# Kernel tuning notes

Measured on AMD Instinct MI355X. Metric: run time of the kernel, lower is better.

The kernel has to match this reference:

```python
import jax, jax.numpy as jnp
import numpy as np

NEG_INF = -1e6  # matches d2l masked_softmax fill value


def masked_softmax(scores, valid_len):
    # scores: [B, Q, K]; valid_len: [B] int — keys at positions >= valid_len[b] are masked
    K = scores.shape[-1]
    mask = jnp.arange(K, dtype=jnp.int32)[None, None, :] < valid_len[:, None, None]
    scores = jnp.where(mask, scores, NEG_INF)
    return jax.nn.softmax(scores, axis=-1)


def setup_inputs() -> dict:
    key = jax.random.key(0)
    k1, k2, k3, k4 = jax.random.split(key, 4)
    B, S, D = 8, 4096, 64
    query = jax.random.normal(k1, (B, S, D), dtype=jnp.float32)
    key_t = jax.random.normal(k2, (B, S, D), dtype=jnp.float32)
    value = jax.random.normal(k3, (B, S, D), dtype=jnp.float32)
    valid_len = jax.random.randint(k4, (B,), 1, S + 1, dtype=jnp.int32)
    return {"query": query, "key": key_t, "value": value, "valid_len": valid_len}


def reference(query, key, value, valid_len):
    d = query.shape[-1]
    # [B, Q, K] score matrix (the module materializes it explicitly)
    scores = jnp.einsum("bqd,bkd->bqk", query, key) / jnp.sqrt(jnp.float32(d))
    attn = masked_softmax(scores, valid_len)
    # dropout p=0.0 (eval): identity
    out = jnp.einsum("bqk,bkd->bqd", attn, value)
    return out
```

## Files before the change

### kernel.cpp

```cpp
#include <hip/hip_runtime.h>
#include <stdint.h>


constexpr int BB = 8;
constexpr int SS = 4096;
constexpr int DH = 64;
constexpr int CH = 32;
constexpr int NKT = SS / CH;
constexpr int TILE_SHORTS = 8192;
constexpr int NTILE = BB * (SS / 128);
constexpr int NSL = 4;
constexpr int SC = NKT / NSL;

typedef short  bfrag  __attribute__((ext_vector_type(8)));
typedef float  f32x16 __attribute__((ext_vector_type(16)));
typedef unsigned int uvec4 __attribute__((ext_vector_type(4)));

__device__ __forceinline__ unsigned short f2bf(float x) {
  unsigned u = __builtin_bit_cast(unsigned, x);
  u += 0x7fffu + ((u >> 16) & 1u);
  return (unsigned short)(u >> 16);
}
__device__ __forceinline__ float bf2f(unsigned short h) {
  return __builtin_bit_cast(float, ((unsigned)h) << 16);
}

__global__ __launch_bounds__(256) void prepack(
    const float* __restrict__ K, const float* __restrict__ V,
    short* __restrict__ ws) {
  const int b  = blockIdx.x >> 7;
  const int kt = blockIdx.x & 127;
  const int t  = threadIdx.x;
  short* tile = ws + (size_t)(b * NKT + kt) * TILE_SHORTS;

  {
    const int d8 = t >> 5, key = t & 31;
    const float* src = K + ((size_t)b * SS + kt * CH + key) * DH + d8 * 8;
    float4 a = ((const float4*)src)[0];
    float4 c = ((const float4*)src)[1];
    float v[8] = {a.x, a.y, a.z, a.w, c.x, c.y, c.z, c.w};
    bfrag hi, lo;
#pragma unroll
    for (int j = 0; j < 8; ++j) {
      unsigned short h = f2bf(v[j]);
      hi[j] = (short)h;
      lo[j] = (short)f2bf(v[j] - bf2f(h));
    }
    *(bfrag*)(tile + t * 8)        = hi;
    *(bfrag*)(tile + 2048 + t * 8) = lo;
  }
  {
    const int k8 = t >> 6, d = t & 63;
    const float* src = V + ((size_t)b * SS + kt * CH + k8 * 8) * DH + d;
    bfrag hi, lo;
#pragma unroll
    for (int j = 0; j < 8; ++j) {
      float x = src[j * DH];
      unsigned short h = f2bf(x);
      hi[j] = (short)h;
      lo[j] = (short)f2bf(x - bf2f(h));
    }
    *(bfrag*)(tile + 4096 + t * 8) = hi;
    *(bfrag*)(tile + 6144 + t * 8) = lo;
  }
}

__global__ __launch_bounds__(256, 4) void attn_mfma(
    const float* __restrict__ Q, const short* __restrict__ wsT,
    const int* __restrict__ VL, float* __restrict__ Out,
    float* __restrict__ part_o, float* __restrict__ part_ml, int nsl, int sc) {
  __shared__ __align__(16) short sKV[2][TILE_SHORTS];

  const int blk = blockIdx.x;
  const int b  = (blk >> 3) & 7;
  const int qs = ((blk >> 6) << 3) | (blk & 7);
  const int qt = qs >> 2;
  const int slice = qs & 3;
  const int tid = threadIdx.x;
  const int w   = tid >> 6;
  const int l   = tid & 63;
  const int hi5 = l >> 5;
  const int l31 = l & 31;

  const int vlen = VL[b];
  const int nch  = (vlen + CH - 1) / CH;
  int nact = (nch + sc - 1) / sc;
  if (nact > nsl) nact = nsl;
  if (slice >= nact) return;
  const int c_lo = slice * sc;
  const int c_hi = min(c_lo + sc, nch);
  const int nchS = c_hi - c_lo;

  bfrag qh[4], ql[4];
  {
    const float* qsrc = Q + ((size_t)b * SS + qt * 128 + w * 32 + l31) * DH;
#pragma unroll
    for (int dt = 0; dt < 4; ++dt) {
      const float* pp = qsrc + dt * 16 + hi5 * 8;
      float4 a = ((const float4*)pp)[0];
      float4 c = ((const float4*)pp)[1];
      float v[8] = {a.x, a.y, a.z, a.w, c.x, c.y, c.z, c.w};
#pragma unroll
      for (int j = 0; j < 8; ++j) {
        float x = v[j] * 0.125f;
        unsigned short h = f2bf(x);
        qh[dt][j] = (short)h;
        ql[dt][j] = (short)f2bf(x - bf2f(h));
      }
    }
  }

  f32x16 o0, o1;
#pragma unroll
  for (int r = 0; r < 16; ++r) { o0[r] = 0.f; o1[r] = 0.f; }
  float m = -1e30f, lsum = 0.f;

  const short* tbase = wsT + (size_t)b * NKT * TILE_SHORTS;

  auto stage = [&](int ci, int buf) {
    const short* g = tbase + (size_t)ci * TILE_SHORTS;
#pragma unroll
    for (int j = 0; j < 4; ++j) {
      __builtin_amdgcn_global_load_lds(
          (const __attribute__((address_space(1))) void*)(g + (j * 256 + tid) * 8),
          (__attribute__((address_space(3))) void*)(&sKV[buf][(j * 256 + tid) * 8]),
          16, 0, 0);
    }
  };

  stage(c_lo, 0);

  for (int t = 0; t < nchS; ++t) {
    __syncthreads();
    const int ci  = c_lo + t;
    const int cur = t & 1;
    if (t + 1 < nchS) stage(ci + 1, cur ^ 1);
    const short* t0 = &sKV[cur][0];

    f32x16 accA, accB;
#pragma unroll
    for (int r = 0; r < 16; ++r) { accA[r] = 0.f; accB[r] = 0.f; }
#pragma unroll
    for (int dt = 0; dt < 4; ++dt) {
      bfrag kh = *(const bfrag*)(t0 + ((2 * dt + hi5) * 32 + l31) * 8);
      bfrag kl = *(const bfrag*)(t0 + 2048 + ((2 * dt + hi5) * 32 + l31) * 8);
      accA = __builtin_amdgcn_mfma_f32_32x32x16_bf16(kh, qh[dt], accA, 0, 0, 0);
      if (dt < 2)
        accA = __builtin_amdgcn_mfma_f32_32x32x16_bf16(kh, ql[dt], accA, 0, 0, 0);
      else
        accB = __builtin_amdgcn_mfma_f32_32x32x16_bf16(kh, ql[dt], accB, 0, 0, 0);
      accB = __builtin_amdgcn_mfma_f32_32x32x16_bf16(kl, qh[dt], accB, 0, 0, 0);
    }
    float s[16];
#pragma unroll
    for (int r = 0; r < 16; ++r) s[r] = accA[r] + accB[r];

    const int c0 = ci * CH;
    if (c0 + CH > vlen) {
#pragma unroll
      for (int r = 0; r < 16; ++r) {
        int key = c0 + (r & 3) + 8 * (r >> 2) + 4 * hi5;
        if (key >= vlen) s[r] = -1e30f;
      }
    }

    float cmax = s[0];
#pragma unroll
    for (int r = 1; r < 16; ++r) cmax = fmaxf(cmax, s[r]);
    cmax = fmaxf(cmax, __shfl_xor(cmax, 32));

    if (__any((int)(cmax > m + 8.0f))) {
      float mn = fmaxf(m, cmax);
      float sc2 = __expf(m - mn);
      m = mn;
      lsum *= sc2;
#pragma unroll
      for (int r = 0; r < 16; ++r) {
        float s2 = __shfl(sc2, (r & 3) + 8 * (r >> 2) + 4 * hi5);
        o0[r] *= s2;
        o1[r] *= s2;
      }
    }

    float ps = 0.f;
#pragma unroll
    for (int r = 0; r < 16; ++r) {
      s[r] = __expf(s[r] - m);
      ps += s[r];
    }
    ps += __shfl_xor(ps, 32);
    lsum += ps;

    unsigned wh[8], wl2[8];
#pragma unroll
    for (int i = 0; i < 8; ++i) {
      float p0 = s[2 * i], p1 = s[2 * i + 1];
      unsigned hw;
      asm("v_cvt_pk_bf16_f32 %0, %1, %2" : "=v"(hw) : "v"(p0), "v"(p1));
      float h0 = __builtin_bit_cast(float, hw << 16);
      float h1 = __builtin_bit_cast(float, hw & 0xffff0000u);
      float r0 = p0 - h0, r1 = p1 - h1;
      unsigned lw;
      asm("v_cvt_pk_bf16_f32 %0, %1, %2" : "=v"(lw) : "v"(r0), "v"(r1));
      wh[i] = hw;
      wl2[i] = lw;
    }
    asm("v_permlane32_swap_b32 %0, %1" : "+v"(wh[0]), "+v"(wh[2]));
    asm("v_permlane32_swap_b32 %0, %1" : "+v"(wh[1]), "+v"(wh[3]));
    asm("v_permlane32_swap_b32 %0, %1" : "+v"(wh[4]), "+v"(wh[6]));
    asm("v_permlane32_swap_b32 %0, %1" : "+v"(wh[5]), "+v"(wh[7]));
    asm("v_permlane32_swap_b32 %0, %1" : "+v"(wl2[0]), "+v"(wl2[2]));
    asm("v_permlane32_swap_b32 %0, %1" : "+v"(wl2[1]), "+v"(wl2[3]));
    asm("v_permlane32_swap_b32 %0, %1" : "+v"(wl2[4]), "+v"(wl2[6]));
    asm("v_permlane32_swap_b32 %0, %1" : "+v"(wl2[5]), "+v"(wl2[7]));
    bfrag ph[2], pl[2];
    {
      uvec4 u0 = {wh[0], wh[1], wh[2], wh[3]};
      uvec4 u1 = {wh[4], wh[5], wh[6], wh[7]};
      uvec4 u2 = {wl2[0], wl2[1], wl2[2], wl2[3]};
      uvec4 u3 = {wl2[4], wl2[5], wl2[6], wl2[7]};
      ph[0] = __builtin_bit_cast(bfrag, u0);
      ph[1] = __builtin_bit_cast(bfrag, u1);
      pl[0] = __builtin_bit_cast(bfrag, u2);
      pl[1] = __builtin_bit_cast(bfrag, u3);
    }

#pragma unroll
    for (int ks = 0; ks < 2; ++ks) {
      const int vo = ((2 * ks + hi5) * 64 + l31) * 8;
      bfrag vh0 = *(const bfrag*)(t0 + 4096 + vo);
      bfrag vl0 = *(const bfrag*)(t0 + 6144 + vo);
      bfrag vh1 = *(const bfrag*)(t0 + 4096 + vo + 256);
      bfrag vl1 = *(const bfrag*)(t0 + 6144 + vo + 256);
      o0 = __builtin_amdgcn_mfma_f32_32x32x16_bf16(ph[ks], vh0, o0, 0, 0, 0);
      o0 = __builtin_amdgcn_mfma_f32_32x32x16_bf16(ph[ks], vl0, o0, 0, 0, 0);
      o0 = __builtin_amdgcn_mfma_f32_32x32x16_bf16(pl[ks], vh0, o0, 0, 0, 0);
      o1 = __builtin_amdgcn_mfma_f32_32x32x16_bf16(ph[ks], vh1, o1, 0, 0, 0);
      o1 = __builtin_amdgcn_mfma_f32_32x32x16_bf16(ph[ks], vl1, o1, 0, 0, 0);
      o1 = __builtin_amdgcn_mfma_f32_32x32x16_bf16(pl[ks], vh1, o1, 0, 0, 0);
    }
  }

  const float linv = 1.0f / lsum;
  if (nact == 1) {
    float* ob = Out + ((size_t)b * SS + qt * 128 + w * 32) * DH;
#pragma unroll
    for (int r = 0; r < 16; ++r) {
      int row = (r & 3) + 8 * (r >> 2) + 4 * hi5;
      float li = __shfl(linv, row);
      ob[row * DH + l31]      = o0[r] * li;
      ob[row * DH + 32 + l31] = o1[r] * li;
    }
  } else {
    const size_t base = (size_t)((b * 32 + qt) * nsl + slice);
    float* po = part_o + base * 8192 + w * 32 * 64;
#pragma unroll
    for (int r = 0; r < 16; ++r) {
      int row = (r & 3) + 8 * (r >> 2) + 4 * hi5;
      po[row * 64 + l31]      = o0[r];
      po[row * 64 + 32 + l31] = o1[r];
    }
    if (hi5 == 0) {
      part_ml[base * 256 + (w * 32 + l31) * 2 + 0] = m;
      part_ml[base * 256 + (w * 32 + l31) * 2 + 1] = lsum;
    }
  }
}

__global__ __launch_bounds__(256) void combine(
    const float* __restrict__ part_o, const float* __restrict__ part_ml,
    const int* __restrict__ VL, float* __restrict__ Out, int nsl, int sc) {
  const int blk = blockIdx.x;
  const int b = blk & 7, qt = blk >> 3;
  const int vlen = VL[b];
  const int nch = (vlen + CH - 1) / CH;
  int nact = (nch + sc - 1) / sc;
  if (nact > nsl) nact = nsl;
  if (nact < 2) return;
  const int row = threadIdx.x >> 1;
  const int seg = (threadIdx.x & 1) * 32;
  const size_t base = (size_t)(b * 32 + qt) * nsl;

  float ms[4], ls[4];
  float M = -1e30f;
#pragma unroll
  for (int s = 0; s < 4; ++s) {
    if (s < nact) {
      ms[s] = part_ml[(base + s) * 256 + row * 2 + 0];
      ls[s] = part_ml[(base + s) * 256 + row * 2 + 1];
      M = fmaxf(M, ms[s]);
    } else { ms[s] = -1e30f; ls[s] = 0.f; }
  }
  float L = 0.f;
#pragma unroll
  for (int s = 0; s < 4; ++s) {
    ms[s] = __expf(ms[s] - M);
    L += ms[s] * ls[s];
  }
  const float linv = 1.0f / L;

  float4 acc[8];
#pragma unroll
  for (int j = 0; j < 8; ++j) acc[j] = make_float4(0.f, 0.f, 0.f, 0.f);
#pragma unroll
  for (int s = 0; s < 4; ++s) {
    if (s < nact) {
      const float4* po =
          (const float4*)(part_o + (base + s) * 8192 + row * 64 + seg);
#pragma unroll
      for (int j = 0; j < 8; ++j) {
        float4 v = po[j];
        acc[j].x += ms[s] * v.x;
        acc[j].y += ms[s] * v.y;
        acc[j].z += ms[s] * v.z;
        acc[j].w += ms[s] * v.w;
      }
    }
  }
  float4* op = (float4*)(Out + ((size_t)b * SS + qt * 128 + row) * DH + seg);
#pragma unroll
  for (int j = 0; j < 8; ++j) {
    acc[j].x *= linv; acc[j].y *= linv; acc[j].z *= linv; acc[j].w *= linv;
    op[j] = acc[j];
  }
}

__global__ __launch_bounds__(256) void attn_naive(
    const float* __restrict__ Q, const float* __restrict__ K,
    const float* __restrict__ V, const int* __restrict__ VL,
    float* __restrict__ Out) {
  const int row = blockIdx.x * 256 + threadIdx.x;
  const int b = row >> 12;
  const int vlen = VL[b];
  const float* q = Q + (size_t)row * DH;
  float qr[DH];
#pragma unroll
  for (int d = 0; d < DH; ++d) qr[d] = q[d] * 0.125f;
  float m = -1e30f, ls = 0.f, o[DH];
#pragma unroll
  for (int d = 0; d < DH; ++d) o[d] = 0.f;
  const float* Kb = K + (size_t)b * SS * DH;
  const float* Vb = V + (size_t)b * SS * DH;
  for (int k = 0; k < vlen; ++k) {
    float sc = 0.f;
    for (int d = 0; d < DH; ++d) sc += qr[d] * Kb[(size_t)k * DH + d];
    if (sc > m) {
      float scale = __expf(m - sc);
      m = sc;
      ls *= scale;
      for (int d = 0; d < DH; ++d) o[d] *= scale;
    }
    float pv = __expf(sc - m);
    ls += pv;
    for (int d = 0; d < DH; ++d) o[d] += pv * Vb[(size_t)k * DH + d];
  }
  for (int d = 0; d < DH; ++d) Out[(size_t)row * DH + d] = o[d] / ls;
}

extern "C" void kernel_launch(void* const* d_in, const int* in_sizes, int n_in,
                              void* d_out, int out_size, void* d_ws,
                              size_t ws_size, hipStream_t stream) {
  const float* Q  = (const float*)d_in[0];
  const float* K  = (const float*)d_in[1];
  const float* V  = (const float*)d_in[2];
  const int*   VL = (const int*)d_in[3];
  float* Out = (float*)d_out;

  const size_t pack_bytes = (size_t)BB * NKT * TILE_SHORTS * sizeof(short);
  const size_t po_bytes   = (size_t)NTILE * NSL * 8192 * sizeof(float);
  const size_t pml_bytes  = (size_t)NTILE * NSL * 256 * sizeof(float);
  const size_t need_split = pack_bytes + po_bytes + pml_bytes;

  if (ws_size >= need_split) {
    short* pack = (short*)d_ws;
    float* po   = (float*)((char*)d_ws + pack_bytes);
    float* pml  = (float*)((char*)d_ws + pack_bytes + po_bytes);
    prepack<<<dim3(BB * NKT), dim3(256), 0, stream>>>(K, V, pack);
    attn_mfma<<<dim3(NTILE * NSL), dim3(256), 0, stream>>>(
        Q, pack, VL, Out, po, pml, NSL, SC);
    combine<<<dim3(NTILE), dim3(256), 0, stream>>>(po, pml, VL, Out, NSL, SC);
  } else if (ws_size >= pack_bytes) {
    short* pack = (short*)d_ws;
    prepack<<<dim3(BB * NKT), dim3(256), 0, stream>>>(K, V, pack);
    attn_mfma<<<dim3(NTILE), dim3(256), 0, stream>>>(
        Q, pack, VL, Out, (float*)d_ws, (float*)d_ws, 1, NKT);
  } else {
    attn_naive<<<dim3(BB * SS / 256), dim3(256), 0, stream>>>(Q, K, V, VL, Out);
  }
}
```

Measured before the change: 171.9 us.

## Balance split-K slices per batch and halve query tile per block

Each batch's valid key chunks are now divided evenly across the four split-K slices, instead of using a fixed slice length that leaves short batches on fewer blocks. The query tile shrinks from 128 to 64 rows, giving 128-thread blocks and twice as many blocks. The combine kernel now always merges all slices, with the partial buffers resized to match. This targets load imbalance from varying valid lengths across batches. In exchange, K/V tiles are streamed twice as often per query row, and the combine pass runs even when splitting is not needed.

```diff
diff --git a/kernel.cpp b/kernel.cpp
--- a/kernel.cpp
+++ b/kernel.cpp
@@ -8,9 +8,8 @@
 constexpr int CH = 32;
 constexpr int NKT = SS / CH;
 constexpr int TILE_SHORTS = 8192;
-constexpr int NTILE = BB * (SS / 128);
+constexpr int TPB = BB * (SS / 64);
 constexpr int NSL = 4;
-constexpr int SC = NKT / NSL;
 
 typedef short  bfrag  __attribute__((ext_vector_type(8)));
 typedef float  f32x16 __attribute__((ext_vector_type(16)));
@@ -65,17 +64,17 @@
   }
 }
 
-__global__ __launch_bounds__(256, 4) void attn_mfma(
+__global__ __launch_bounds__(128, 4) void attn_mfma(
     const float* __restrict__ Q, const short* __restrict__ wsT,
     const int* __restrict__ VL, float* __restrict__ Out,
-    float* __restrict__ part_o, float* __restrict__ part_ml, int nsl, int sc) {
+    float* __restrict__ part_o, float* __restrict__ part_ml, int nsl) {
   __shared__ __align__(16) short sKV[2][TILE_SHORTS];
 
   const int blk = blockIdx.x;
-  const int b  = (blk >> 3) & 7;
-  const int qs = ((blk >> 6) << 3) | (blk & 7);
-  const int qt = qs >> 2;
-  const int slice = qs & 3;
+  const int b    = blk & 7;
+  const int rest = blk >> 3;
+  const int qt    = rest / nsl;
+  const int slice = rest % nsl;
   const int tid = threadIdx.x;
   const int w   = tid >> 6;
   const int l   = tid & 63;
@@ -84,16 +83,13 @@
 
   const int vlen = VL[b];
   const int nch  = (vlen + CH - 1) / CH;
-  int nact = (nch + sc - 1) / sc;
-  if (nact > nsl) nact = nsl;
-  if (slice >= nact) return;
-  const int c_lo = slice * sc;
-  const int c_hi = min(c_lo + sc, nch);
+  const int c_lo = slice * nch / nsl;
+  const int c_hi = (slice + 1) * nch / nsl;
   const int nchS = c_hi - c_lo;
 
   bfrag qh[4], ql[4];
   {
-    const float* qsrc = Q + ((size_t)b * SS + qt * 128 + w * 32 + l31) * DH;
+    const float* qsrc = Q + ((size_t)b * SS + qt * 64 + w * 32 + l31) * DH;
 #pragma unroll
     for (int dt = 0; dt < 4; ++dt) {
       const float* pp = qsrc + dt * 16 + hi5 * 8;
@@ -120,15 +116,15 @@
   auto stage = [&](int ci, int buf) {
     const short* g = tbase + (size_t)ci * TILE_SHORTS;
 #pragma unroll
-    for (int j = 0; j < 4; ++j) {
+    for (int j = 0; j < 8; ++j) {
       __builtin_amdgcn_global_load_lds(
-          (const __attribute__((address_space(1))) void*)(g + (j * 256 + tid) * 8),
-          (__attribute__((address_space(3))) void*)(&sKV[buf][(j * 256 + tid) * 8]),
+          (const __attribute__((address_space(1))) void*)(g + (j * 128 + tid) * 8),
+          (__attribute__((address_space(3))) void*)(&sKV[buf][(j * 128 + tid) * 8]),
           16, 0, 0);
     }
   };
 
-  stage(c_lo, 0);
+  if (nchS > 0) stage(c_lo, 0);
 
   for (int t = 0; t < nchS; ++t) {
     __syncthreads();
@@ -241,9 +237,9 @@
     }
   }
 
-  const float linv = 1.0f / lsum;
-  if (nact == 1) {
-    float* ob = Out + ((size_t)b * SS + qt * 128 + w * 32) * DH;
+  if (nsl == 1) {
+    const float linv = 1.0f / lsum;
+    float* ob = Out + ((size_t)b * SS + qt * 64 + w * 32) * DH;
 #pragma unroll
     for (int r = 0; r < 16; ++r) {
       int row = (r & 3) + 8 * (r >> 2) + 4 * hi5;
@@ -252,8 +248,8 @@
       ob[row * DH + 32 + l31] = o1[r] * li;
     }
   } else {
-    const size_t base = (size_t)((b * 32 + qt) * nsl + slice);
-    float* po = part_o + base * 8192 + w * 32 * 64;
+    const size_t base = (size_t)((b * 64 + qt) * nsl + slice);
+    float* po = part_o + base * 4096 + w * 32 * 64;
 #pragma unroll
     for (int r = 0; r < 16; ++r) {
       int row = (r & 3) + 8 * (r >> 2) + 4 * hi5;
@@ -261,65 +257,56 @@
       po[row * 64 + 32 + l31] = o1[r];
     }
     if (hi5 == 0) {
-      part_ml[base * 256 + (w * 32 + l31) * 2 + 0] = m;
-      part_ml[base * 256 + (w * 32 + l31) * 2 + 1] = lsum;
+      part_ml[base * 128 + (w * 32 + l31) * 2 + 0] = m;
+      part_ml[base * 128 + (w * 32 + l31) * 2 + 1] = lsum;
     }
   }
 }
 
 __global__ __launch_bounds__(256) void combine(
     const float* __restrict__ part_o, const float* __restrict__ part_ml,
-    const int* __restrict__ VL, float* __restrict__ Out, int nsl, int sc) {
+    float* __restrict__ Out, int nsl) {
   const int blk = blockIdx.x;
   const int b = blk & 7, qt = blk >> 3;
-  const int vlen = VL[b];
-  const int nch = (vlen + CH - 1) / CH;
-  int nact = (nch + sc - 1) / sc;
-  if (nact > nsl) nact = nsl;
-  if (nact < 2) return;
-  const int row = threadIdx.x >> 1;
-  const int seg = (threadIdx.x & 1) * 32;
-  const size_t base = (size_t)(b * 32 + qt) * nsl;
-
-  float ms[4], ls[4];
+  const int row = threadIdx.x >> 2;
+  const int seg = (threadIdx.x & 3) * 16;
+  const size_t base = (size_t)(b * 64 + qt) * nsl;
+
+  float ms[NSL], ls[NSL];
   float M = -1e30f;
 #pragma unroll
-  for (int s = 0; s < 4; ++s) {
-    if (s < nact) {
-      ms[s] = part_ml[(base + s) * 256 + row * 2 + 0];
-      ls[s] = part_ml[(base + s) * 256 + row * 2 + 1];
-      M = fmaxf(M, ms[s]);
-    } else { ms[s] = -1e30f; ls[s] = 0.f; }
+  for (int s = 0; s < NSL; ++s) {
+    ms[s] = part_ml[(base + s) * 128 + row * 2 + 0];
+    ls[s] = part_ml[(base + s) * 128 + row * 2 + 1];
+    M = fmaxf(M, ms[s]);
   }
   float L = 0.f;
 #pragma unroll
-  for (int s = 0; s < 4; ++s) {
+  for (int s = 0; s < NSL; ++s) {
     ms[s] = __expf(ms[s] - M);
     L += ms[s] * ls[s];
   }
   const float linv = 1.0f / L;
 
-  float4 acc[8];
-#pragma unroll
-  for (int j = 0; j < 8; ++j) acc[j] = make_float4(0.f, 0.f, 0.f, 0.f);
-#pragma unroll
-  for (int s = 0; s < 4; ++s) {
-    if (s < nact) {
-      const float4* po =
-          (const float4*)(part_o + (base + s) * 8192 + row * 64 + seg);
-#pragma unroll
-      for (int j = 0; j < 8; ++j) {
-        float4 v = po[j];
-        acc[j].x += ms[s] * v.x;
-        acc[j].y += ms[s] * v.y;
-        acc[j].z += ms[s] * v.z;
-        acc[j].w += ms[s] * v.w;
-      }
-    }
-  }
-  float4* op = (float4*)(Out + ((size_t)b * SS + qt * 128 + row) * DH + seg);
-#pragma unroll
-  for (int j = 0; j < 8; ++j) {
+  float4 acc[4];
+#pragma unroll
+  for (int j = 0; j < 4; ++j) acc[j] = make_float4(0.f, 0.f, 0.f, 0.f);
+#pragma unroll
+  for (int s = 0; s < NSL; ++s) {
+    const float4* po =
+        (const float4*)(part_o + (base + s) * 4096 + row * 64 + seg);
+#pragma unroll
+    for (int j = 0; j < 4; ++j) {
+      float4 v = po[j];
+      acc[j].x += ms[s] * v.x;
+      acc[j].y += ms[s] * v.y;
+      acc[j].z += ms[s] * v.z;
+      acc[j].w += ms[s] * v.w;
+    }
+  }
+  float4* op = (float4*)(Out + ((size_t)b * SS + qt * 64 + row) * DH + seg);
+#pragma unroll
+  for (int j = 0; j < 4; ++j) {
     acc[j].x *= linv; acc[j].y *= linv; acc[j].z *= linv; acc[j].w *= linv;
     op[j] = acc[j];
   }
@@ -367,8 +354,8 @@
   float* Out = (float*)d_out;
 
   const size_t pack_bytes = (size_t)BB * NKT * TILE_SHORTS * sizeof(short);
-  const size_t po_bytes   = (size_t)NTILE * NSL * 8192 * sizeof(float);
-  const size_t pml_bytes  = (size_t)NTILE * NSL * 256 * sizeof(float);
+  const size_t po_bytes   = (size_t)TPB * NSL * 4096 * sizeof(float);
+  const size_t pml_bytes  = (size_t)TPB * NSL * 128 * sizeof(float);
   const size_t need_split = pack_bytes + po_bytes + pml_bytes;
 
   if (ws_size >= need_split) {
@@ -376,14 +363,14 @@
     float* po   = (float*)((char*)d_ws + pack_bytes);
     float* pml  = (float*)((char*)d_ws + pack_bytes + po_bytes);
     prepack<<<dim3(BB * NKT), dim3(256), 0, stream>>>(K, V, pack);
-    attn_mfma<<<dim3(NTILE * NSL), dim3(256), 0, stream>>>(
-        Q, pack, VL, Out, po, pml, NSL, SC);
-    combine<<<dim3(NTILE), dim3(256), 0, stream>>>(po, pml, VL, Out, NSL, SC);
+    attn_mfma<<<dim3(TPB * NSL), dim3(128), 0, stream>>>(
+        Q, pack, VL, Out, po, pml, NSL);
+    combine<<<dim3(TPB), dim3(256), 0, stream>>>(po, pml, Out, NSL);
   } else if (ws_size >= pack_bytes) {
     short* pack = (short*)d_ws;
     prepack<<<dim3(BB * NKT), dim3(256), 0, stream>>>(K, V, pack);
-    attn_mfma<<<dim3(NTILE), dim3(256), 0, stream>>>(
-        Q, pack, VL, Out, (float*)d_ws, (float*)d_ws, 1, NKT);
+    attn_mfma<<<dim3(TPB), dim3(128), 0, stream>>>(
+        Q, pack, VL, Out, (float*)d_ws, (float*)d_ws, 1);
   } else {
     attn_naive<<<dim3(BB * SS / 256), dim3(256), 0, stream>>>(Q, K, V, VL, Out);
   }
```

New measurement: 186.4 us. 8.5% more time.

## Split valid key range evenly across slices and raise MFMA wave priority

Applied to the files above, without the earlier changes.

The split-K scheme used to give each slice a fixed chunk range, so batches with short valid lengths used fewer slices and loaded CUs unevenly. Each slice now takes an equal share of that batch's valid chunks, and the combine always merges all NSL partials. s_setprio is also raised around the MFMA sections to help waves in their matrix phase issue first. An empty slice (nch < nsl) writes m=-1e30 and l=0, which the combine tolerates, but the combine now always reads every partial even when one slice would have been enough.

```diff
diff --git a/kernel.cpp b/kernel.cpp
--- a/kernel.cpp
+++ b/kernel.cpp
@@ -10,7 +10,6 @@
 constexpr int TILE_SHORTS = 8192;
 constexpr int NTILE = BB * (SS / 128);
 constexpr int NSL = 4;
-constexpr int SC = NKT / NSL;
 
 typedef short  bfrag  __attribute__((ext_vector_type(8)));
 typedef float  f32x16 __attribute__((ext_vector_type(16)));
@@ -68,7 +67,7 @@
 __global__ __launch_bounds__(256, 4) void attn_mfma(
     const float* __restrict__ Q, const short* __restrict__ wsT,
     const int* __restrict__ VL, float* __restrict__ Out,
-    float* __restrict__ part_o, float* __restrict__ part_ml, int nsl, int sc) {
+    float* __restrict__ part_o, float* __restrict__ part_ml, int nsl) {
   __shared__ __align__(16) short sKV[2][TILE_SHORTS];
 
   const int blk = blockIdx.x;
@@ -84,11 +83,8 @@
 
   const int vlen = VL[b];
   const int nch  = (vlen + CH - 1) / CH;
-  int nact = (nch + sc - 1) / sc;
-  if (nact > nsl) nact = nsl;
-  if (slice >= nact) return;
-  const int c_lo = slice * sc;
-  const int c_hi = min(c_lo + sc, nch);
+  const int c_lo = slice * nch / nsl;
+  const int c_hi = (slice + 1) * nch / nsl;
   const int nchS = c_hi - c_lo;
 
   bfrag qh[4], ql[4];
@@ -128,7 +124,7 @@
     }
   };
 
-  stage(c_lo, 0);
+  if (nchS > 0) stage(c_lo, 0);
 
   for (int t = 0; t < nchS; ++t) {
     __syncthreads();
@@ -140,6 +136,7 @@
     f32x16 accA, accB;
 #pragma unroll
     for (int r = 0; r < 16; ++r) { accA[r] = 0.f; accB[r] = 0.f; }
+    __builtin_amdgcn_s_setprio(1);
 #pragma unroll
     for (int dt = 0; dt < 4; ++dt) {
       bfrag kh = *(const bfrag*)(t0 + ((2 * dt + hi5) * 32 + l31) * 8);
@@ -151,6 +148,7 @@
         accB = __builtin_amdgcn_mfma_f32_32x32x16_bf16(kh, ql[dt], accB, 0, 0, 0);
       accB = __builtin_amdgcn_mfma_f32_32x32x16_bf16(kl, qh[dt], accB, 0, 0, 0);
     }
+    __builtin_amdgcn_s_setprio(0);
     float s[16];
 #pragma unroll
     for (int r = 0; r < 16; ++r) s[r] = accA[r] + accB[r];
@@ -225,6 +223,7 @@
       pl[1] = __builtin_bit_cast(bfrag, u3);
     }
 
+    __builtin_amdgcn_s_setprio(1);
 #pragma unroll
     for (int ks = 0; ks < 2; ++ks) {
       const int vo = ((2 * ks + hi5) * 64 + l31) * 8;
@@ -239,10 +238,11 @@
       o1 = __builtin_amdgcn_mfma_f32_32x32x16_bf16(ph[ks], vl1, o1, 0, 0, 0);
       o1 = __builtin_amdgcn_mfma_f32_32x32x16_bf16(pl[ks], vh1, o1, 0, 0, 0);
     }
-  }
-
-  const float linv = 1.0f / lsum;
-  if (nact == 1) {
+    __builtin_amdgcn_s_setprio(0);
+  }
+
+  if (nsl == 1) {
+    const float linv = 1.0f / lsum;
     float* ob = Out + ((size_t)b * SS + qt * 128 + w * 32) * DH;
 #pragma unroll
     for (int r = 0; r < 16; ++r) {
@@ -269,31 +269,24 @@
 
 __global__ __launch_bounds__(256) void combine(
     const float* __restrict__ part_o, const float* __restrict__ part_ml,
-    const int* __restrict__ VL, float* __restrict__ Out, int nsl, int sc) {
+    float* __restrict__ Out) {
   const int blk = blockIdx.x;
   const int b = blk & 7, qt = blk >> 3;
-  const int vlen = VL[b];
-  const int nch = (vlen + CH - 1) / CH;
-  int nact = (nch + sc - 1) / sc;
-  if (nact > nsl) nact = nsl;
-  if (nact < 2) return;
   const int row = threadIdx.x >> 1;
   const int seg = (threadIdx.x & 1) * 32;
-  const size_t base = (size_t)(b * 32 + qt) * nsl;
-
-  float ms[4], ls[4];
+  const size_t base = (size_t)(b * 32 + qt) * NSL;
+
+  float ms[NSL], ls[NSL];
   float M = -1e30f;
 #pragma unroll
-  for (int s = 0; s < 4; ++s) {
-    if (s < nact) {
-      ms[s] = part_ml[(base + s) * 256 + row * 2 + 0];
-      ls[s] = part_ml[(base + s) * 256 + row * 2 + 1];
-      M = fmaxf(M, ms[s]);
-    } else { ms[s] = -1e30f; ls[s] = 0.f; }
+  for (int s = 0; s < NSL; ++s) {
+    ms[s] = part_ml[(base + s) * 256 + row * 2 + 0];
+    ls[s] = part_ml[(base + s) * 256 + row * 2 + 1];
+    M = fmaxf(M, ms[s]);
   }
   float L = 0.f;
 #pragma unroll
-  for (int s = 0; s < 4; ++s) {
+  for (int s = 0; s < NSL; ++s) {
     ms[s] = __expf(ms[s] - M);
     L += ms[s] * ls[s];
   }
@@ -303,18 +296,16 @@
 #pragma unroll
   for (int j = 0; j < 8; ++j) acc[j] = make_float4(0.f, 0.f, 0.f, 0.f);
 #pragma unroll
-  for (int s = 0; s < 4; ++s) {
-    if (s < nact) {
-      const float4* po =
-          (const float4*)(part_o + (base + s) * 8192 + row * 64 + seg);
-#pragma unroll
-      for (int j = 0; j < 8; ++j) {
-        float4 v = po[j];
-        acc[j].x += ms[s] * v.x;
-        acc[j].y += ms[s] * v.y;
-        acc[j].z += ms[s] * v.z;
-        acc[j].w += ms[s] * v.w;
-      }
+  for (int s = 0; s < NSL; ++s) {
+    const float4* po =
+        (const float4*)(part_o + (base + s) * 8192 + row * 64 + seg);
+#pragma unroll
+    for (int j = 0; j < 8; ++j) {
+      float4 v = po[j];
+      acc[j].x += ms[s] * v.x;
+      acc[j].y += ms[s] * v.y;
+      acc[j].z += ms[s] * v.z;
+      acc[j].w += ms[s] * v.w;
     }
   }
   float4* op = (float4*)(Out + ((size_t)b * SS + qt * 128 + row) * DH + seg);
@@ -377,13 +368,13 @@
     float* pml  = (float*)((char*)d_ws + pack_bytes + po_bytes);
     prepack<<<dim3(BB * NKT), dim3(256), 0, stream>>>(K, V, pack);
     attn_mfma<<<dim3(NTILE * NSL), dim3(256), 0, stream>>>(
-        Q, pack, VL, Out, po, pml, NSL, SC);
-    combine<<<dim3(NTILE), dim3(256), 0, stream>>>(po, pml, VL, Out, NSL, SC);
+        Q, pack, VL, Out, po, pml, NSL);
+    combine<<<dim3(NTILE), dim3(256), 0, stream>>>(po, pml, Out);
   } else if (ws_size >= pack_bytes) {
     short* pack = (short*)d_ws;
     prepack<<<dim3(BB * NKT), dim3(256), 0, stream>>>(K, V, pack);
     attn_mfma<<<dim3(NTILE), dim3(256), 0, stream>>>(
-        Q, pack, VL, Out, (float*)d_ws, (float*)d_ws, 1, NKT);
+        Q, pack, VL, Out, (float*)d_ws, (float*)d_ws, 1);
   } else {
     attn_naive<<<dim3(BB * SS / 256), dim3(256), 0, stream>>>(Q, K, V, VL, Out);
   }
```

Result: slower. 179.3 us (+4.3%).
